# Kernel tuning notes

Hardware: AMD Instinct MI355X
Metric: run time of the kernel (lower is better)

## Reference

```python
import jax, jax.numpy as jnp
import numpy as np
from jax import lax

_EPS = 1e-6
N_POINTS = 2048


def quat_to_rot(q):
    # q = (x, y, z, w), same convention as quaternion_to_rotation_matrix_torch
    # (its analytic Jacobians dR/dq in the kernel match this unnormalized form)
    x, y, z, w = q[0], q[1], q[2], q[3]
    return jnp.stack([
        jnp.stack([1 - 2 * (y * y + z * z), 2 * (x * y - z * w), 2 * (x * z + y * w)]),
        jnp.stack([2 * (x * y + z * w), 1 - 2 * (x * x + z * z), 2 * (y * z - x * w)]),
        jnp.stack([2 * (x * z - y * w), 2 * (y * z + x * w), 1 - 2 * (x * x + y * y)]),
    ])


def setup_inputs() -> dict:
    key = jax.random.key(0)
    ks = jax.random.split(key, 8)
    H, W = 512, 512
    # points in front of camera, projecting inside the image
    z = jax.random.uniform(ks[0], (N_POINTS, 1), minval=2.0, maxval=6.0)
    xy_dir = jax.random.uniform(ks[1], (N_POINTS, 2), minval=-0.45, maxval=0.45)
    pointcloud = jnp.concatenate([xy_dir * z, z], axis=1)  # [N,3]
    point_color = jax.random.uniform(ks[2], (N_POINTS, 3))
    point_alpha = jax.random.uniform(ks[3], (N_POINTS,), minval=0.1, maxval=0.9)
    # conic = inverse 2x2 covariance in pixel space, stored (a, b, c):
    ac = jax.random.uniform(ks[4], (N_POINTS, 2), minval=0.02, maxval=0.10)
    b = jax.random.uniform(ks[5], (N_POINTS, 1), minval=-0.01, maxval=0.01)
    point_conic = jnp.concatenate([ac[:, :1], b, ac[:, 1:]], axis=1)  # [N,3]
    # near-identity camera pose (x,y,z,w quaternion)
    q = jnp.array([0.01, -0.02, 0.015, 1.0], dtype=jnp.float32)
    q_pointcloud_camera = q / jnp.linalg.norm(q)
    t_pointcloud_camera = 0.05 * jax.random.normal(ks[6], (3,), dtype=jnp.float32)
    fx = fy = 500.0
    camera_intrinsics = jnp.array([[fx, 0.0, W / 2.0], [0.0, fy, H / 2.0], [0.0, 0.0, 1.0]], dtype=jnp.float32)
    return {
        "pointcloud": pointcloud.astype(jnp.float32),
        "point_color": point_color.astype(jnp.float32),
        "point_alpha": point_alpha.astype(jnp.float32),
        "point_conic": point_conic.astype(jnp.float32),
        "q_pointcloud_camera": q_pointcloud_camera,
        "t_pointcloud_camera": t_pointcloud_camera,
        "camera_intrinsics": camera_intrinsics,
        "camera_height": H,
        "camera_width": W,
    }


def _rasterize(pointcloud, point_color, point_alpha, point_conic, q, t, K, H, W):
    R = quat_to_rot(q)
    p_cam = pointcloud @ R.T + t  # [N,3] camera-frame positions
    depth = p_cam[:, 2]
    proj = p_cam @ K.T
    uv = proj[:, :2] / (depth[:, None] + _EPS)  # [N,2] pixel coords
    # depth sort (front-to-back), matching the sorted per-tile traversal
    order = jnp.argsort(depth)
    uv_s = uv[order]
    conic_s = point_conic[order]
    col_s = point_color[order]
    a_s = point_alpha[order]
    d_s = depth[order]

    px = jnp.arange(W, dtype=jnp.float32) + 0.5  # pixel centers, as in kernel
    py = jnp.arange(H, dtype=jnp.float32) + 0.5

    def step(carry, xs):
        T, rgb, dacc = carry
        uv_i, conic_i, col_i, a_i, d_i = xs
        dx = px[None, :] - uv_i[0]  # [1,W] -> broadcast [H,W]
        dy = py[:, None] - uv_i[1]  # [H,1]
        power = -0.5 * (conic_i[0] * dx * dx + 2.0 * conic_i[1] * dx * dy + conic_i[2] * dy * dy)
        g = jnp.exp(jnp.minimum(power, 0.0))  # gaussian density in [0,1]
        prod = g * a_i
        alpha = jnp.where(prod >= 1.0 / 255.0, jnp.minimum(prod, 0.99), 0.0)
        w = T * alpha
        rgb = rgb + w[..., None] * col_i
        dacc = dacc + w * d_i
        T = T * (1.0 - alpha)
        return (T, rgb, dacc), None

    carry0 = (jnp.ones((H, W), jnp.float32), jnp.zeros((H, W, 3), jnp.float32), jnp.zeros((H, W), jnp.float32))
    (T, rgb, dacc), _ = lax.scan(step, carry0, (uv_s, conic_s, col_s, a_s, d_s))
    # [H,W,5] = rgb, rasterized_depth, accumulated_alpha
    return jnp.concatenate([rgb, dacc[..., None], (1.0 - T)[..., None]], axis=-1)


def reference(pointcloud, point_color, point_alpha, point_conic, q_pointcloud_camera, t_pointcloud_camera, camera_intrinsics, camera_height, camera_width):
    return _rasterize(pointcloud, point_color, point_alpha, point_conic,
                      q_pointcloud_camera, t_pointcloud_camera, camera_intrinsics,
                      camera_height, camera_width)
```

## Files before the change

### kernel.cpp

```cpp
#include <hip/hip_runtime.h>
#include <math.h>

#define NPTS 2048
#define IMG_W 512
#define IMG_H 512
#define RW 16
#define RH 32
#define NBX (IMG_W / RW)
#define NBY (IMG_H / RH)
#define NTHREADS 256
#define NCHUNK (NPTS / NTHREADS)
#define CAP 256
#define RSTRIDE 12

__global__ __launch_bounds__(NTHREADS) void gs_fused(
    const float* __restrict__ pc,
    const float* __restrict__ col,
    const float* __restrict__ alp,
    const float* __restrict__ con,
    const float* __restrict__ q,
    const float* __restrict__ t,
    const float* __restrict__ K,
    float* __restrict__ out) {
  __shared__ float s_pts[CAP * RSTRIDE];
  __shared__ unsigned long long s_key[CAP];
  __shared__ int s_total;

  int tid = threadIdx.x;
  if (tid == 0) s_total = 0;
  int rx = (blockIdx.x % NBX) * RW;
  int ry = (blockIdx.x / NBX) * RH;
  int lx = tid & 15, ly = tid >> 4;
  float px = rx + lx + 0.5f;
  float py0 = ry + ly + 0.5f;
  float tx0 = rx + 0.5f, tx1 = rx + RW - 0.5f;
  float ty0 = ry + 0.5f, ty1 = ry + RH - 0.5f;

  float qx = q[0], qy = q[1], qz = q[2], qw = q[3];
  float r00 = 1.f - 2.f * (qy * qy + qz * qz), r01 = 2.f * (qx * qy - qz * qw),
        r02 = 2.f * (qx * qz + qy * qw);
  float r10 = 2.f * (qx * qy + qz * qw), r11 = 1.f - 2.f * (qx * qx + qz * qz),
        r12 = 2.f * (qy * qz - qx * qw);
  float r20 = 2.f * (qx * qz - qy * qw), r21 = 2.f * (qy * qz + qx * qw),
        r22 = 1.f - 2.f * (qx * qx + qy * qy);
  float t0 = t[0], t1 = t[1], t2 = t[2];
  float fx = K[0], cx = K[2], fy = K[4], cy = K[5];

#define PROJ(i, ux, uy, Z)                      \
  float ux, uy, Z;                              \
  {                                             \
    float x = pc[3 * (i)], y = pc[3 * (i) + 1], \
          z = pc[3 * (i) + 2];                  \
    Z = r20 * x + r21 * y + r22 * z + t2;       \
    float X = r00 * x + r01 * y + r02 * z + t0; \
    float Y = r10 * x + r11 * y + r12 * z + t1; \
    float inv = 1.0f / (Z + 1e-6f);             \
    ux = (fx * X + cx * Z) * inv;               \
    uy = (fy * Y + cy * Z) * inv;               \
  }

  __syncthreads();

#pragma unroll
  for (int c = 0; c < NCHUNK; c++) {
    int i = c * NTHREADS + tid;
    PROJ(i, ux, uy, Z);
    float A = con[3 * i], B = con[3 * i + 1], C = con[3 * i + 2];
    float a = alp[i];
    float th = 2.0f * __logf(255.0f * a);
    float absB = fabsf(B);
    float dxm = fmaxf(0.0f, fmaxf(tx0 - ux, ux - tx1));
    float dym = fmaxf(0.0f, fmaxf(ty0 - uy, uy - ty1));
    float bound =
        fmaxf(A - absB, 0.0f) * dxm * dxm + fmaxf(C - absB, 0.0f) * dym * dym;
    if (bound <= th + 1e-3f) {
      int slot = atomicAdd(&s_total, 1);
      if (slot < CAP) {
        float4* d = (float4*)(s_pts + (size_t)slot * RSTRIDE);
        d[0] = {ux, uy, A, B};
        d[1] = {C, a, Z, th};
        d[2] = {col[3 * i], col[3 * i + 1], col[3 * i + 2], 0.0f};
        s_key[slot] =
            ((unsigned long long)__float_as_uint(Z) << 32) | (unsigned)i;
      }
    }
  }
  __syncthreads();
  int total = s_total;

  float T0 = 1.0f, ar0 = 0.f, ag0 = 0.f, ab0 = 0.f, ad0 = 0.f;
  float T1 = 1.0f, ar1 = 0.f, ag1 = 0.f, ab1 = 0.f, ad1 = 0.f;

#define COMPOSITE2(w0, w1, w2)                                   \
  {                                                              \
    float dx = px - w0.x;                                        \
    float dy0 = py0 - w0.y, dy1 = dy0 + 16.0f;                   \
    float adx2 = w0.z * dx * dx;                                 \
    float bdx2 = 2.0f * w0.w * dx;                               \
    float pw0 = -0.5f * (adx2 + bdx2 * dy0 + w1.x * dy0 * dy0);  \
    float pw1 = -0.5f * (adx2 + bdx2 * dy1 + w1.x * dy1 * dy1);  \
    float g0 = __expf(fminf(pw0, 0.0f));                         \
    float g1 = __expf(fminf(pw1, 0.0f));                         \
    float prod0 = g0 * w1.y, prod1 = g1 * w1.y;                  \
    if (prod0 >= (1.0f / 255.0f)) {                              \
      float al = fminf(prod0, 0.99f);                            \
      float w = T0 * al;                                         \
      ar0 += w * w2.x; ag0 += w * w2.y; ab0 += w * w2.z;         \
      ad0 += w * w1.z;                                           \
      T0 *= (1.0f - al);                                         \
    }                                                            \
    if (prod1 >= (1.0f / 255.0f)) {                              \
      float al = fminf(prod1, 0.99f);                            \
      float w = T1 * al;                                         \
      ar1 += w * w2.x; ag1 += w * w2.y; ab1 += w * w2.z;         \
      ad1 += w * w1.z;                                           \
      T1 *= (1.0f - al);                                         \
    }                                                            \
  }

  if (total <= CAP) {
    bool have = tid < total;
    unsigned long long myk = 0;
    float4 ra, rb, rc;
    int pos = 0;
    if (have) {
      myk = s_key[tid];
      const float4* s = (const float4*)(s_pts + (size_t)tid * RSTRIDE);
      ra = s[0]; rb = s[1]; rc = s[2];
      for (int j = 0; j < total; j++) pos += (s_key[j] < myk);
    }
    __syncthreads();
    if (have) {
      float4* d = (float4*)(s_pts + (size_t)pos * RSTRIDE);
      d[0] = ra; d[1] = rb; d[2] = rc;
    }
    __syncthreads();

    for (int kk = 0; kk < total; kk++) {
      const float4* p4 = (const float4*)(s_pts + (size_t)kk * RSTRIDE);
      float4 w0 = p4[0], w1 = p4[1], w2 = p4[2];
      COMPOSITE2(w0, w1, w2);
    }
  } else {
    float dep[NCHUNK];
    unsigned live = 0;
#pragma unroll
    for (int c = 0; c < NCHUNK; c++) {
      int i = c * NTHREADS + tid;
      PROJ(i, ux, uy, Z);
      dep[c] = Z;
      float A = con[3 * i], B = con[3 * i + 1], C = con[3 * i + 2];
      float th = 2.0f * __logf(255.0f * alp[i]);
      float absB = fabsf(B);
      float dxm = fmaxf(0.0f, fmaxf(tx0 - ux, ux - tx1));
      float dym = fmaxf(0.0f, fmaxf(ty0 - uy, uy - ty1));
      float bound = fmaxf(A - absB, 0.0f) * dxm * dxm +
                    fmaxf(C - absB, 0.0f) * dym * dym;
      live |= (unsigned)(bound <= th + 1e-3f) << c;
    }
    __syncthreads();
    float* s_rd = s_pts;
    int* s_ro = (int*)(s_pts + NTHREADS);
    float* s_rec = s_pts + 2 * NTHREADS;
    while (1) {
      float bd = 1e30f;
      int bo = 0x7fffffff;
#pragma unroll
      for (int c = 0; c < NCHUNK; c++) {
        if ((live >> c) & 1) {
          int o = c * NTHREADS + tid;
          if (dep[c] < bd || (dep[c] == bd && o < bo)) { bd = dep[c]; bo = o; }
        }
      }
      s_rd[tid] = bd;
      s_ro[tid] = bo;
      __syncthreads();
      float wd = 1e30f;
      int wo = 0x7fffffff;
      for (int j = 0; j < NTHREADS; j++) {
        float d = s_rd[j];
        int o = s_ro[j];
        if (d < wd || (d == wd && o < wo)) { wd = d; wo = o; }
      }
      __syncthreads();
      if (wo == 0x7fffffff) break;
      if (tid == (wo & (NTHREADS - 1))) {
        int i = wo;
        PROJ(i, ux, uy, Z);
        float a = alp[i];
        float4* d = (float4*)s_rec;
        d[0] = {ux, uy, con[3 * i], con[3 * i + 1]};
        d[1] = {con[3 * i + 2], a, Z, 0.0f};
        d[2] = {col[3 * i], col[3 * i + 1], col[3 * i + 2], 0.0f};
        live &= ~(1u << (wo / NTHREADS));
      }
      __syncthreads();
      float4 w0 = ((float4*)s_rec)[0], w1 = ((float4*)s_rec)[1],
             w2 = ((float4*)s_rec)[2];
      COMPOSITE2(w0, w1, w2);
    }
  }
#undef COMPOSITE2
#undef PROJ

  int o0 = ((ry + ly) * IMG_W + (rx + lx)) * 5;
  int o1 = ((ry + ly + 16) * IMG_W + (rx + lx)) * 5;
  out[o0 + 0] = ar0;
  out[o0 + 1] = ag0;
  out[o0 + 2] = ab0;
  out[o0 + 3] = ad0;
  out[o0 + 4] = 1.0f - T0;
  out[o1 + 0] = ar1;
  out[o1 + 1] = ag1;
  out[o1 + 2] = ab1;
  out[o1 + 3] = ad1;
  out[o1 + 4] = 1.0f - T1;
}

extern "C" void kernel_launch(void* const* d_in, const int* in_sizes, int n_in,
                              void* d_out, int out_size, void* d_ws,
                              size_t ws_size, hipStream_t stream) {
  const float* pc = (const float*)d_in[0];
  const float* col = (const float*)d_in[1];
  const float* alp = (const float*)d_in[2];
  const float* con = (const float*)d_in[3];
  const float* q = (const float*)d_in[4];
  const float* t = (const float*)d_in[5];
  const float* K = (const float*)d_in[6];
  float* out = (float*)d_out;

  gs_fused<<<NBX * NBY, NTHREADS, 0, stream>>>(pc, col, alp, con, q, t, K,
                                               out);
}
```

Before: 16.99 us.

## Pack color and depth as fp16 in shared records and make compositing branchless

Shrinks each shared-memory splat record from 12 to 8 floats by storing RGB and depth as packed half pairs, so the per-splat compositing loop does two LDS vector loads instead of three. The per-pixel blend is also rewritten to be branchless, with alpha set to zero when below threshold. This cuts LDS traffic and divergence in the hot loop, at the cost of fp16 rounding of color and depth (depth values 2-6 lose precision) and extra conversion instructions.

```diff
diff --git a/kernel.cpp b/kernel.cpp
--- a/kernel.cpp
+++ b/kernel.cpp
@@ -1,4 +1,5 @@
 #include <hip/hip_runtime.h>
+#include <hip/hip_fp16.h>
 #include <math.h>
 
 #define NPTS 2048
@@ -11,7 +12,20 @@
 #define NTHREADS 256
 #define NCHUNK (NPTS / NTHREADS)
 #define CAP 256
-#define RSTRIDE 12
+#define RSTRIDE 8
+
+typedef __fp16 f16x2 __attribute__((ext_vector_type(2)));
+
+static __device__ __forceinline__ float pack2h(float a, float b) {
+  union { f16x2 h; float f; } u;
+  u.h = __builtin_amdgcn_cvt_pkrtz(a, b);
+  return u.f;
+}
+static __device__ __forceinline__ float2 unpack2h(float f) {
+  unsigned u = __float_as_uint(f);
+  return {__half2float(__ushort_as_half((unsigned short)(u & 0xffff))),
+          __half2float(__ushort_as_half((unsigned short)(u >> 16)))};
+}
 
 __global__ __launch_bounds__(NTHREADS) void gs_fused(
     const float* __restrict__ pc,
@@ -78,8 +92,8 @@
       if (slot < CAP) {
         float4* d = (float4*)(s_pts + (size_t)slot * RSTRIDE);
         d[0] = {ux, uy, A, B};
-        d[1] = {C, a, Z, th};
-        d[2] = {col[3 * i], col[3 * i + 1], col[3 * i + 2], 0.0f};
+        d[1] = {C, a, pack2h(col[3 * i], col[3 * i + 1]),
+                pack2h(col[3 * i + 2], Z)};
         s_key[slot] =
             ((unsigned long long)__float_as_uint(Z) << 32) | (unsigned)i;
       }
@@ -91,55 +105,55 @@
   float T0 = 1.0f, ar0 = 0.f, ag0 = 0.f, ab0 = 0.f, ad0 = 0.f;
   float T1 = 1.0f, ar1 = 0.f, ag1 = 0.f, ab1 = 0.f, ad1 = 0.f;
 
-#define COMPOSITE2(w0, w1, w2)                                   \
+#define COMPOSITE2(w0, w1)                                       \
   {                                                              \
     float dx = px - w0.x;                                        \
     float dy0 = py0 - w0.y, dy1 = dy0 + 16.0f;                   \
     float adx2 = w0.z * dx * dx;                                 \
     float bdx2 = 2.0f * w0.w * dx;                               \
-    float pw0 = -0.5f * (adx2 + bdx2 * dy0 + w1.x * dy0 * dy0);  \
-    float pw1 = -0.5f * (adx2 + bdx2 * dy1 + w1.x * dy1 * dy1);  \
+    float Cc = w1.x, aa = w1.y;                                  \
+    float2 rg = unpack2h(w1.z);                                  \
+    float2 bZ = unpack2h(w1.w);                                  \
+    float pw0 = -0.5f * (adx2 + bdx2 * dy0 + Cc * dy0 * dy0);    \
+    float pw1 = -0.5f * (adx2 + bdx2 * dy1 + Cc * dy1 * dy1);    \
     float g0 = __expf(fminf(pw0, 0.0f));                         \
     float g1 = __expf(fminf(pw1, 0.0f));                         \
-    float prod0 = g0 * w1.y, prod1 = g1 * w1.y;                  \
-    if (prod0 >= (1.0f / 255.0f)) {                              \
-      float al = fminf(prod0, 0.99f);                            \
-      float w = T0 * al;                                         \
-      ar0 += w * w2.x; ag0 += w * w2.y; ab0 += w * w2.z;         \
-      ad0 += w * w1.z;                                           \
-      T0 *= (1.0f - al);                                         \
-    }                                                            \
-    if (prod1 >= (1.0f / 255.0f)) {                              \
-      float al = fminf(prod1, 0.99f);                            \
-      float w = T1 * al;                                         \
-      ar1 += w * w2.x; ag1 += w * w2.y; ab1 += w * w2.z;         \
-      ad1 += w * w1.z;                                           \
-      T1 *= (1.0f - al);                                         \
-    }                                                            \
+    float prod0 = g0 * aa, prod1 = g1 * aa;                      \
+    float al0 =                                                  \
+        (prod0 >= (1.0f / 255.0f)) ? fminf(prod0, 0.99f) : 0.0f; \
+    float al1 =                                                  \
+        (prod1 >= (1.0f / 255.0f)) ? fminf(prod1, 0.99f) : 0.0f; \
+    float w0_ = T0 * al0, w1_ = T1 * al1;                        \
+    ar0 += w0_ * rg.x; ag0 += w0_ * rg.y;                        \
+    ab0 += w0_ * bZ.x; ad0 += w0_ * bZ.y;                        \
+    T0 *= (1.0f - al0);                                          \
+    ar1 += w1_ * rg.x; ag1 += w1_ * rg.y;                        \
+    ab1 += w1_ * bZ.x; ad1 += w1_ * bZ.y;                        \
+    T1 *= (1.0f - al1);                                          \
   }
 
   if (total <= CAP) {
     bool have = tid < total;
     unsigned long long myk = 0;
-    float4 ra, rb, rc;
+    float4 ra, rb;
     int pos = 0;
     if (have) {
       myk = s_key[tid];
       const float4* s = (const float4*)(s_pts + (size_t)tid * RSTRIDE);
-      ra = s[0]; rb = s[1]; rc = s[2];
+      ra = s[0]; rb = s[1];
       for (int j = 0; j < total; j++) pos += (s_key[j] < myk);
     }
     __syncthreads();
     if (have) {
       float4* d = (float4*)(s_pts + (size_t)pos * RSTRIDE);
-      d[0] = ra; d[1] = rb; d[2] = rc;
+      d[0] = ra; d[1] = rb;
     }
     __syncthreads();
 
     for (int kk = 0; kk < total; kk++) {
       const float4* p4 = (const float4*)(s_pts + (size_t)kk * RSTRIDE);
-      float4 w0 = p4[0], w1 = p4[1], w2 = p4[2];
-      COMPOSITE2(w0, w1, w2);
+      float4 w0 = p4[0], w1 = p4[1];
+      COMPOSITE2(w0, w1);
     }
   } else {
     float dep[NCHUNK];
@@ -190,14 +204,13 @@
         float a = alp[i];
         float4* d = (float4*)s_rec;
         d[0] = {ux, uy, con[3 * i], con[3 * i + 1]};
-        d[1] = {con[3 * i + 2], a, Z, 0.0f};
-        d[2] = {col[3 * i], col[3 * i + 1], col[3 * i + 2], 0.0f};
+        d[1] = {con[3 * i + 2], a, pack2h(col[3 * i], col[3 * i + 1]),
+                pack2h(col[3 * i + 2], Z)};
         live &= ~(1u << (wo / NTHREADS));
       }
       __syncthreads();
-      float4 w0 = ((float4*)s_rec)[0], w1 = ((float4*)s_rec)[1],
-             w2 = ((float4*)s_rec)[2];
-      COMPOSITE2(w0, w1, w2);
+      float4 w0 = ((float4*)s_rec)[0], w1 = ((float4*)s_rec)[1];
+      COMPOSITE2(w0, w1);
     }
   }
 #undef COMPOSITE2
```

New measurement: 16.70 us. No clear change (-1.7%).
